# Kernel tuning notes

Hardware: AMD Instinct MI355X
Metric: run time of the kernel (lower is better)

## Reference

```python
import jax, jax.numpy as jnp
import numpy as np


def _conv3x3(x, w, stride=1):
    # x: [N, C_in, H, W], w: [C_out, C_in, 3, 3] (ternary {-1,0,1}), padding=1, no bias
    return jax.lax.conv_general_dilated(
        x, w,
        window_strides=(stride, stride),
        padding=((1, 1), (1, 1)),
        dimension_numbers=("NCHW", "OIHW", "NCHW"),
    )


def _bn(x, gamma, beta, mean, var, eps=1e-5):
    # inference-mode BatchNorm2d over channel dim
    inv = gamma * jax.lax.rsqrt(var + eps)
    return x * inv[None, :, None, None] + (beta - mean * inv)[None, :, None, None]


def setup_inputs() -> dict:
    key = jax.random.key(0)
    ks = jax.random.split(key, 8)
    N, C, H, W = 64, 256, 32, 32
    x = jax.random.normal(ks[0], (N, C, H, W), dtype=jnp.float32)
    # Ternary conv weights in {-1, 0, +1} (scale_and_shift=False => raw ternary values)
    w1 = jax.random.randint(ks[1], (C, C, 3, 3), -1, 2).astype(jnp.float32)
    w2 = jax.random.randint(ks[2], (C, C, 3, 3), -1, 2).astype(jnp.float32)
    # BatchNorm affine params and running stats
    g1 = jax.random.normal(ks[3], (C,), dtype=jnp.float32) * 0.1 + 1.0
    b1 = jax.random.normal(ks[4], (C,), dtype=jnp.float32) * 0.1
    g2 = jax.random.normal(ks[5], (C,), dtype=jnp.float32) * 0.1 + 1.0
    b2 = jax.random.normal(ks[6], (C,), dtype=jnp.float32) * 0.1
    rm1 = jnp.zeros((C,), dtype=jnp.float32)
    rv1 = jnp.ones((C,), dtype=jnp.float32)
    rm2 = jnp.zeros((C,), dtype=jnp.float32)
    rv2 = jnp.ones((C,), dtype=jnp.float32)
    return {"x": x, "w1": w1, "g1": g1, "b1": b1, "rm1": rm1, "rv1": rv1,
            "w2": w2, "g2": g2, "b2": b2, "rm2": rm2, "rv2": rv2}


def reference(x, w1, g1, b1, rm1, rv1, w2, g2, b2, rm2, rv2):
    # BasicBlock forward: stride=1, downsample=None -> identity skip
    h = _conv3x3(x, w1, stride=1)
    h = _bn(h, g1, b1, rm1, rv1)
    h = jax.nn.relu(h)
    h = _conv3x3(h, w2, stride=1)
    h = _bn(h, g2, b2, rm2, rv2)
    return jax.nn.relu(x + h)
```

## Files before the change

### kernel.cpp

```cpp
#include <hip/hip_runtime.h>

typedef unsigned short u16;
typedef unsigned int u32;
typedef __attribute__((ext_vector_type(8))) short bf16x8;
typedef __attribute__((ext_vector_type(4))) float f32x4;

__device__ __forceinline__ u16 f2bf(float f) {
    u32 u = __float_as_uint(f);
    u += 0x7fffu + ((u >> 16) & 1u);
    return (u16)(u >> 16);
}

__device__ __forceinline__ void llds16(void* l, const void* g) {
    __builtin_amdgcn_global_load_lds(
        (const __attribute__((address_space(1))) u32*)g,
        (__attribute__((address_space(3))) u32*)l, 16, 0, 0);
}

__global__ void prep(const float* __restrict__ x, u16* __restrict__ xt,
                     const float* __restrict__ w1, const float* __restrict__ w2,
                     u16* __restrict__ W1t, u16* __restrict__ W2t,
                     const float* __restrict__ g1, const float* __restrict__ b1,
                     const float* __restrict__ rm1, const float* __restrict__ rv1,
                     const float* __restrict__ g2, const float* __restrict__ b2,
                     const float* __restrict__ rm2, const float* __restrict__ rv2,
                     float* __restrict__ sc, u32* __restrict__ zp) {
    int t = threadIdx.x;
    int b = blockIdx.x;
    if (b < 16384) {
        __shared__ float xl[32 * 33];
        int n = b >> 8, rem = b & 255;
        int h = rem >> 3, c0 = (rem & 7) << 5;
        int cl = t >> 5, w = t & 31;
#pragma unroll
        for (int i = 0; i < 4; ++i) {
            int c = c0 + i * 8 + cl;
            xl[(i * 8 + cl) * 33 + w] = x[(n * 256 + c) * 1024 + h * 32 + w];
        }
        __syncthreads();
        int wo = t >> 3, k = t & 7;
        ushort4 o;
        o.x = f2bf(xl[(k * 4 + 0) * 33 + wo]);
        o.y = f2bf(xl[(k * 4 + 1) * 33 + wo]);
        o.z = f2bf(xl[(k * 4 + 2) * 33 + wo]);
        o.w = f2bf(xl[(k * 4 + 3) * 33 + wo]);
        *(ushort4*)&xt[((n * 32 + h) * 32 + wo) * 256 + c0 + k * 4] = o;
    } else {
        int bb = b - 16384;
        int idx = (bb & 255) * 256 + t;
        const float* src = (bb >> 8) ? w2 : w1;
        u16* dst = (bb >> 8) ? W2t : W1t;
        const float* s = src + idx * 9;
        int co = idx >> 8, ci = idx & 255;
#pragma unroll
        for (int p = 0; p < 9; ++p)
            dst[p * 65536 + co * 256 + ci] = f2bf(s[p]);
        if (bb == 0) {
            float s1 = g1[t] * rsqrtf(rv1[t] + 1e-5f);
            sc[t]       = s1;
            sc[256 + t] = b1[t] - rm1[t] * s1;
            float s2 = g2[t] * rsqrtf(rv2[t] + 1e-5f);
            sc[512 + t] = s2;
            sc[768 + t] = b2[t] - rm2[t] * s2;
            zp[t] = 0u;
            zp[t + 256] = 0u;
        }
    }
}

__global__ __launch_bounds__(256, 1) void conv_mfma(
    const u16* __restrict__ Xt,
    const u16* __restrict__ Wt,
    const float* __restrict__ sv,
    const float* __restrict__ tv,
    const float* __restrict__ skip,
    u16* __restrict__ ybf,
    float* __restrict__ yf,
    const u16* __restrict__ zp, int stage)
{
    __shared__ alignas(16) u16 ldsA[2][9 * 4 * 64 * 8];
    __shared__ alignas(16) u16 ldsB[2][40 * 64 * 8];

    int t = threadIdx.x;
    int wv = t >> 6, lane = t & 63;
    int q = lane >> 4, n16 = lane & 15;

    int bid = blockIdx.x;
    int co_t = (bid >> 3) & 3;
    int sp   = ((bid >> 5) << 3) | (bid & 7);
    int h_t  = sp & 1, nb = sp >> 1;
    int co0 = co_t << 6, h0 = h_t << 4;

    const u16* aSrc[9];
#pragma unroll
    for (int i = 0; i < 9; ++i) {
        int g = wv * 9 + i;
        int p = g >> 2, mt = g & 3;
        aSrc[i] = Wt + (p << 16) + ((co0 + (mt << 4) + n16) << 8) + (q << 3);
    }
    const u16* bSrc[10];
#pragma unroll
    for (int j = 0; j < 10; ++j) {
        int g2 = wv * 10 + j;
        int s = g2 * 64 + lane;
        int hi = s / 136, rem = s - hi * 136;
        int wp = rem >> 2, qq = rem & 3;
        int hin = h0 - 1 + hi;
        bool v = (wp >= 1) && (wp <= 32) && (hin >= 0) && (hin < 32);
        bSrc[j] = v ? (Xt + (((nb << 5) + hin) * 32 + (wp - 1)) * 256 + (qq << 3))
                    : (zp + lane * 8);
    }

    f32x4 acc[4][8] = {};

#pragma unroll
    for (int i = 0; i < 9; ++i)
        llds16(&ldsA[0][(wv * 9 + i) << 9], aSrc[i]);
#pragma unroll
    for (int j = 0; j < 10; ++j)
        llds16(&ldsB[0][(wv * 10 + j) << 9], bSrc[j]);

    int c = 0;
    for (int kt = 0; kt < 8; ++kt) {
        if (kt < 7) {
            int kc = (kt + 1) << 5;
#pragma unroll
            for (int i = 0; i < 9; ++i)
                llds16(&ldsA[c ^ 1][(wv * 9 + i) << 9], aSrc[i] + kc);
#pragma unroll
            for (int j = 0; j < 10; ++j)
                llds16(&ldsB[c ^ 1][(wv * 10 + j) << 9], bSrc[j] + kc);
            asm volatile("s_waitcnt vmcnt(19)" ::: "memory");
        } else {
            asm volatile("s_waitcnt vmcnt(0)" ::: "memory");
        }
        __builtin_amdgcn_s_barrier();
        __builtin_amdgcn_sched_barrier(0);

        const u16* pA = ldsA[c];
        const u16* pB = ldsB[c];
        __builtin_amdgcn_s_setprio(1);
#pragma unroll
        for (int kw = 0; kw < 3; ++kw) {
            bf16x8 bFr[6][2];
#pragma unroll
            for (int r = 0; r < 6; ++r)
#pragma unroll
                for (int half = 0; half < 2; ++half) {
                    int hi = (wv << 2) + r;
                    int wp = (half << 4) + n16 + kw;
                    bFr[r][half] = *(const bf16x8*)
                        &pB[(hi * 136 + (wp << 2) + q) << 3];
                }
#pragma unroll
            for (int kh = 0; kh < 3; ++kh) {
                int p = kh * 3 + kw;
                bf16x8 aF[4];
#pragma unroll
                for (int mt = 0; mt < 4; ++mt)
                    aF[mt] = *(const bf16x8*)&pA[((p << 8) + (mt << 6) + lane) << 3];
#pragma unroll
                for (int mt = 0; mt < 4; ++mt)
#pragma unroll
                    for (int nt = 0; nt < 8; ++nt)
                        acc[mt][nt] = __builtin_amdgcn_mfma_f32_16x16x32_bf16(
                            aF[mt], bFr[(nt >> 1) + kh][nt & 1], acc[mt][nt], 0, 0, 0);
            }
        }
        __builtin_amdgcn_s_setprio(0);
        __builtin_amdgcn_sched_barrier(0);
        __builtin_amdgcn_s_barrier();
        c ^= 1;
    }

    if (stage == 1) {
#pragma unroll
        for (int mt = 0; mt < 4; ++mt) {
            int cb = co0 + (mt << 4) + (q << 2);
            f32x4 ss = *(const f32x4*)&sv[cb];
            f32x4 tt = *(const f32x4*)&tv[cb];
#pragma unroll
            for (int nt = 0; nt < 8; ++nt) {
                int h = h0 + (wv << 2) + (nt >> 1), w = ((nt & 1) << 4) + n16;
                ushort4 o;
                o.x = f2bf(fmaxf(acc[mt][nt][0] * ss[0] + tt[0], 0.f));
                o.y = f2bf(fmaxf(acc[mt][nt][1] * ss[1] + tt[1], 0.f));
                o.z = f2bf(fmaxf(acc[mt][nt][2] * ss[2] + tt[2], 0.f));
                o.w = f2bf(fmaxf(acc[mt][nt][3] * ss[3] + tt[3], 0.f));
                *(ushort4*)&ybf[(((nb << 5) + h) * 32 + w) * 256 + cb] = o;
            }
        }
    } else {
#pragma unroll
        for (int mt = 0; mt < 4; ++mt) {
            int cb = co0 + (mt << 4) + (q << 2);
            f32x4 ss = *(const f32x4*)&sv[cb];
            f32x4 tt = *(const f32x4*)&tv[cb];
#pragma unroll
            for (int nt = 0; nt < 8; ++nt) {
                int h = h0 + (wv << 2) + (nt >> 1), w = ((nt & 1) << 4) + n16;
#pragma unroll
                for (int j = 0; j < 4; ++j) {
                    int idx = (((nb << 8) + cb + j) << 10) + (h << 5) + w;
                    yf[idx] = fmaxf(acc[mt][nt][j] * ss[j] + tt[j] + skip[idx], 0.f);
                }
            }
        }
    }
}

extern "C" void kernel_launch(void* const* d_in, const int* in_sizes, int n_in,
                              void* d_out, int out_size, void* d_ws, size_t ws_size,
                              hipStream_t stream) {
    const float* x   = (const float*)d_in[0];
    const float* w1  = (const float*)d_in[1];
    const float* g1  = (const float*)d_in[2];
    const float* b1  = (const float*)d_in[3];
    const float* rm1 = (const float*)d_in[4];
    const float* rv1 = (const float*)d_in[5];
    const float* w2  = (const float*)d_in[6];
    const float* g2  = (const float*)d_in[7];
    const float* b2  = (const float*)d_in[8];
    const float* rm2 = (const float*)d_in[9];
    const float* rv2 = (const float*)d_in[10];

    char* ws = (char*)d_ws;
    u16*  XT  = (u16*)(ws);
    u16*  H1  = (u16*)(ws + 33554432);
    u16*  W1t = (u16*)(ws + 67108864);
    u16*  W2t = (u16*)(ws + 68288512);
    float* sc = (float*)(ws + 69468160);
    u32*  zpg = (u32*)(ws + 69472256);
    if (ws_size < 69474304) return;

    prep<<<16896, 256, 0, stream>>>(x, XT, w1, w2, W1t, W2t,
                                    g1, b1, rm1, rv1, g2, b2, rm2, rv2,
                                    sc, zpg);

    conv_mfma<<<512, 256, 0, stream>>>(XT, W1t, sc, sc + 256, nullptr,
                                       H1, nullptr, (const u16*)zpg, 1);
    conv_mfma<<<512, 256, 0, stream>>>(H1, W2t, sc + 512, sc + 768, x,
                                       nullptr, (float*)d_out, (const u16*)zpg, 2);
}
```

Measured before the change: 306.7 us.

## Double waves per conv block and split global-to-LDS loads by wave role

Each conv block now runs 512 threads (8 waves) in place of 256. Every wave covers 2 output rows instead of 4, which halves the accumulator array and the B-fragment registers per wave. The global-to-LDS copies are split by role: waves 0-3 load the input tile (10 loads each) and waves 4-7 load the weight tile (9 loads each), with the vmcnt waits adjusted to match. The aim is more waves to hide latency and fewer registers per wave. The cost is more barrier participants, and the A fragments are now loaded from LDS twice as often relative to the MFMA work.

```diff
diff --git a/kernel.cpp b/kernel.cpp
--- a/kernel.cpp
+++ b/kernel.cpp
@@ -68,7 +68,7 @@
     }
 }
 
-__global__ __launch_bounds__(256, 1) void conv_mfma(
+__global__ __launch_bounds__(512, 1) void conv_mfma(
     const u16* __restrict__ Xt,
     const u16* __restrict__ Wt,
     const float* __restrict__ sv,
@@ -91,46 +91,53 @@
     int h_t  = sp & 1, nb = sp >> 1;
     int co0 = co_t << 6, h0 = h_t << 4;
 
-    const u16* aSrc[9];
-#pragma unroll
-    for (int i = 0; i < 9; ++i) {
-        int g = wv * 9 + i;
-        int p = g >> 2, mt = g & 3;
-        aSrc[i] = Wt + (p << 16) + ((co0 + (mt << 4) + n16) << 8) + (q << 3);
-    }
-    const u16* bSrc[10];
-#pragma unroll
-    for (int j = 0; j < 10; ++j) {
-        int g2 = wv * 10 + j;
-        int s = g2 * 64 + lane;
-        int hi = s / 136, rem = s - hi * 136;
-        int wp = rem >> 2, qq = rem & 3;
-        int hin = h0 - 1 + hi;
-        bool v = (wp >= 1) && (wp <= 32) && (hin >= 0) && (hin < 32);
-        bSrc[j] = v ? (Xt + (((nb << 5) + hin) * 32 + (wp - 1)) * 256 + (qq << 3))
-                    : (zp + lane * 8);
-    }
-
-    f32x4 acc[4][8] = {};
-
-#pragma unroll
-    for (int i = 0; i < 9; ++i)
-        llds16(&ldsA[0][(wv * 9 + i) << 9], aSrc[i]);
-#pragma unroll
-    for (int j = 0; j < 10; ++j)
-        llds16(&ldsB[0][(wv * 10 + j) << 9], bSrc[j]);
+    const u16* src[10];
+    u32 dstOff[10];
+    bool isB = (wv < 4);
+    int nld = isB ? 10 : 9;
+    if (isB) {
+#pragma unroll
+        for (int j = 0; j < 10; ++j) {
+            int g2 = wv * 10 + j;
+            int s = g2 * 64 + lane;
+            int hi = s / 136, rem = s - hi * 136;
+            int wp = rem >> 2, qq = rem & 3;
+            int hin = h0 - 1 + hi;
+            bool v = (wp >= 1) && (wp <= 32) && (hin >= 0) && (hin < 32);
+            src[j] = v ? (Xt + (((nb << 5) + hin) * 32 + (wp - 1)) * 256 + (qq << 3))
+                       : (zp + lane * 8);
+            dstOff[j] = (u32)g2 << 9;
+        }
+    } else {
+#pragma unroll
+        for (int i = 0; i < 9; ++i) {
+            int g = (wv - 4) * 9 + i;
+            int p = g >> 2, mt = g & 3;
+            src[i] = Wt + (p << 16) + ((co0 + (mt << 4) + n16) << 8) + (q << 3);
+            dstOff[i] = (u32)g << 9;
+        }
+        src[9] = zp; dstOff[9] = 0;
+    }
+
+    f32x4 acc[4][4] = {};
+
+    {
+        u16* dst = isB ? ldsB[0] : ldsA[0];
+#pragma unroll
+        for (int j = 0; j < 10; ++j)
+            if (j < nld) llds16(&dst[dstOff[j]], src[j]);
+    }
 
     int c = 0;
     for (int kt = 0; kt < 8; ++kt) {
         if (kt < 7) {
             int kc = (kt + 1) << 5;
-#pragma unroll
-            for (int i = 0; i < 9; ++i)
-                llds16(&ldsA[c ^ 1][(wv * 9 + i) << 9], aSrc[i] + kc);
+            u16* dst = isB ? ldsB[c ^ 1] : ldsA[c ^ 1];
 #pragma unroll
             for (int j = 0; j < 10; ++j)
-                llds16(&ldsB[c ^ 1][(wv * 10 + j) << 9], bSrc[j] + kc);
-            asm volatile("s_waitcnt vmcnt(19)" ::: "memory");
+                if (j < nld) llds16(&dst[dstOff[j]], src[j] + kc);
+            if (isB) asm volatile("s_waitcnt vmcnt(10)" ::: "memory");
+            else     asm volatile("s_waitcnt vmcnt(9)"  ::: "memory");
         } else {
             asm volatile("s_waitcnt vmcnt(0)" ::: "memory");
         }
@@ -142,12 +149,12 @@
         __builtin_amdgcn_s_setprio(1);
 #pragma unroll
         for (int kw = 0; kw < 3; ++kw) {
-            bf16x8 bFr[6][2];
-#pragma unroll
-            for (int r = 0; r < 6; ++r)
+            bf16x8 bFr[4][2];
+#pragma unroll
+            for (int r = 0; r < 4; ++r)
 #pragma unroll
                 for (int half = 0; half < 2; ++half) {
-                    int hi = (wv << 2) + r;
+                    int hi = (wv << 1) + r;
                     int wp = (half << 4) + n16 + kw;
                     bFr[r][half] = *(const bf16x8*)
                         &pB[(hi * 136 + (wp << 2) + q) << 3];
@@ -162,7 +169,7 @@
 #pragma unroll
                 for (int mt = 0; mt < 4; ++mt)
 #pragma unroll
-                    for (int nt = 0; nt < 8; ++nt)
+                    for (int nt = 0; nt < 4; ++nt)
                         acc[mt][nt] = __builtin_amdgcn_mfma_f32_16x16x32_bf16(
                             aF[mt], bFr[(nt >> 1) + kh][nt & 1], acc[mt][nt], 0, 0, 0);
             }
@@ -180,8 +187,8 @@
             f32x4 ss = *(const f32x4*)&sv[cb];
             f32x4 tt = *(const f32x4*)&tv[cb];
 #pragma unroll
-            for (int nt = 0; nt < 8; ++nt) {
-                int h = h0 + (wv << 2) + (nt >> 1), w = ((nt & 1) << 4) + n16;
+            for (int nt = 0; nt < 4; ++nt) {
+                int h = h0 + (wv << 1) + (nt >> 1), w = ((nt & 1) << 4) + n16;
                 ushort4 o;
                 o.x = f2bf(fmaxf(acc[mt][nt][0] * ss[0] + tt[0], 0.f));
                 o.y = f2bf(fmaxf(acc[mt][nt][1] * ss[1] + tt[1], 0.f));
@@ -197,8 +204,8 @@
             f32x4 ss = *(const f32x4*)&sv[cb];
             f32x4 tt = *(const f32x4*)&tv[cb];
 #pragma unroll
-            for (int nt = 0; nt < 8; ++nt) {
-                int h = h0 + (wv << 2) + (nt >> 1), w = ((nt & 1) << 4) + n16;
+            for (int nt = 0; nt < 4; ++nt) {
+                int h = h0 + (wv << 1) + (nt >> 1), w = ((nt & 1) << 4) + n16;
 #pragma unroll
                 for (int j = 0; j < 4; ++j) {
                     int idx = (((nb << 8) + cb + j) << 10) + (h << 5) + w;
@@ -237,8 +244,8 @@
                                     g1, b1, rm1, rv1, g2, b2, rm2, rv2,
                                     sc, zpg);
 
-    conv_mfma<<<512, 256, 0, stream>>>(XT, W1t, sc, sc + 256, nullptr,
+    conv_mfma<<<512, 512, 0, stream>>>(XT, W1t, sc, sc + 256, nullptr,
                                        H1, nullptr, (const u16*)zpg, 1);
-    conv_mfma<<<512, 256, 0, stream>>>(H1, W2t, sc + 512, sc + 768, x,
+    conv_mfma<<<512, 512, 0, stream>>>(H1, W2t, sc + 512, sc + 768, x,
                                        nullptr, (float*)d_out, (const u16*)zpg, 2);
 }
```

New measurement: 272.6 us. 11.1% less time.

## Use full-height 512-thread tiles with wave-specialized A/B loaders

Applied to the files above, without the earlier changes.

Each block now computes all 32 output rows of one image for 64 output channels with 8 waves, which halves the grid and cuts redundant halo loads of the input tile. Waves 0-3 load weights (double-buffered) and waves 4-7 load the activation tile. The activation tile is single-buffered: the kw=2 fragments are prefetched into registers so the next chunk can be loaded mid-iteration. The risks are weaker load/compute overlap from the vmcnt(0) wait at the top of each iteration, and register pressure. Launch bounds of (512,2) may cap VGPRs low enough to spill the 128-float accumulator.

```diff
diff --git a/kernel.cpp b/kernel.cpp
--- a/kernel.cpp
+++ b/kernel.cpp
@@ -68,7 +68,7 @@
     }
 }
 
-__global__ __launch_bounds__(256, 1) void conv_mfma(
+__global__ __launch_bounds__(512, 2) void conv_mfma(
     const u16* __restrict__ Xt,
     const u16* __restrict__ Wt,
     const float* __restrict__ sv,
@@ -79,7 +79,7 @@
     const u16* __restrict__ zp, int stage)
 {
     __shared__ alignas(16) u16 ldsA[2][9 * 4 * 64 * 8];
-    __shared__ alignas(16) u16 ldsB[2][40 * 64 * 8];
+    __shared__ alignas(16) u16 ldsB[73 * 512];
 
     int t = threadIdx.x;
     int wv = t >> 6, lane = t & 63;
@@ -87,78 +87,79 @@
 
     int bid = blockIdx.x;
     int co_t = (bid >> 3) & 3;
-    int sp   = ((bid >> 5) << 3) | (bid & 7);
-    int h_t  = sp & 1, nb = sp >> 1;
-    int co0 = co_t << 6, h0 = h_t << 4;
-
-    const u16* aSrc[9];
-#pragma unroll
-    for (int i = 0; i < 9; ++i) {
-        int g = wv * 9 + i;
-        int p = g >> 2, mt = g & 3;
-        aSrc[i] = Wt + (p << 16) + ((co0 + (mt << 4) + n16) << 8) + (q << 3);
-    }
-    const u16* bSrc[10];
-#pragma unroll
-    for (int j = 0; j < 10; ++j) {
-        int g2 = wv * 10 + j;
-        int s = g2 * 64 + lane;
-        int hi = s / 136, rem = s - hi * 136;
-        int wp = rem >> 2, qq = rem & 3;
-        int hin = h0 - 1 + hi;
-        bool v = (wp >= 1) && (wp <= 32) && (hin >= 0) && (hin < 32);
-        bSrc[j] = v ? (Xt + (((nb << 5) + hin) * 32 + (wp - 1)) * 256 + (qq << 3))
-                    : (zp + lane * 8);
+    int n = (bid & 7) | ((bid >> 5) << 3);
+    int co0 = co_t << 6;
+
+    bool isA = (wv < 4);
+    u32 srcOff[19];
+    if (isA) {
+#pragma unroll
+        for (int i = 0; i < 9; ++i) {
+            int g = wv * 9 + i;
+            int p = g >> 2, mt = g & 3;
+            srcOff[i] = (u32)((p << 16) + ((co0 + (mt << 4) + n16) << 8) + (q << 3));
+        }
+    } else {
+        u32 zpOff = (u32)((const u16*)zp - Xt);
+#pragma unroll
+        for (int j = 0; j < 19; ++j) {
+            int g2 = (wv - 4) + 4 * j;
+            int s = g2 * 64 + lane;
+            int hi = s / 136, rem = s - hi * 136;
+            int wp = rem >> 2, qq = rem & 3;
+            int h = hi - 1, w = wp - 1;
+            bool v = (s < 4624) && (h >= 0) && (h < 32) && (w >= 0) && (w < 32);
+            srcOff[j] = v ? (u32)(((n * 32 + h) * 32 + w) * 256 + (qq << 3))
+                          : (zpOff + lane * 8);
+        }
     }
 
     f32x4 acc[4][8] = {};
 
-#pragma unroll
-    for (int i = 0; i < 9; ++i)
-        llds16(&ldsA[0][(wv * 9 + i) << 9], aSrc[i]);
-#pragma unroll
-    for (int j = 0; j < 10; ++j)
-        llds16(&ldsB[0][(wv * 10 + j) << 9], bSrc[j]);
+    if (isA) {
+#pragma unroll
+        for (int i = 0; i < 9; ++i)
+            llds16((char*)&ldsA[0][0] + (((u32)(wv * 9 + i)) << 10), Xt ? (Wt + srcOff[i]) : 0);
+    } else {
+#pragma unroll
+        for (int j = 0; j < 18; ++j)
+            llds16((char*)ldsB + (((u32)((wv - 4) + 4 * j)) << 10), Xt + srcOff[j]);
+        if (wv == 4)
+            llds16((char*)ldsB + (72u << 10), Xt + srcOff[18]);
+    }
 
     int c = 0;
     for (int kt = 0; kt < 8; ++kt) {
-        if (kt < 7) {
-            int kc = (kt + 1) << 5;
+        asm volatile("s_waitcnt vmcnt(0)" ::: "memory");
+        __builtin_amdgcn_s_barrier();
+
+        const u16* pA = ldsA[c];
+        int kc1 = (kt + 1) << 5;
+        if (kt < 7 && isA) {
 #pragma unroll
             for (int i = 0; i < 9; ++i)
-                llds16(&ldsA[c ^ 1][(wv * 9 + i) << 9], aSrc[i] + kc);
-#pragma unroll
-            for (int j = 0; j < 10; ++j)
-                llds16(&ldsB[c ^ 1][(wv * 10 + j) << 9], bSrc[j] + kc);
-            asm volatile("s_waitcnt vmcnt(19)" ::: "memory");
-        } else {
-            asm volatile("s_waitcnt vmcnt(0)" ::: "memory");
-        }
-        __builtin_amdgcn_s_barrier();
+                llds16((char*)&ldsA[c ^ 1][0] + (((u32)(wv * 9 + i)) << 10),
+                       Wt + srcOff[i] + kc1);
+        }
         __builtin_amdgcn_sched_barrier(0);
 
-        const u16* pA = ldsA[c];
-        const u16* pB = ldsB[c];
-        __builtin_amdgcn_s_setprio(1);
-#pragma unroll
-        for (int kw = 0; kw < 3; ++kw) {
+#pragma unroll
+        for (int kw = 0; kw < 2; ++kw) {
             bf16x8 bFr[6][2];
 #pragma unroll
-            for (int r = 0; r < 6; ++r)
-#pragma unroll
-                for (int half = 0; half < 2; ++half) {
-                    int hi = (wv << 2) + r;
-                    int wp = (half << 4) + n16 + kw;
-                    bFr[r][half] = *(const bf16x8*)
-                        &pB[(hi * 136 + (wp << 2) + q) << 3];
-                }
+            for (int rr = 0; rr < 6; ++rr)
+#pragma unroll
+                for (int half = 0; half < 2; ++half)
+                    bFr[rr][half] = *(const bf16x8*)
+                        &ldsB[(((wv * 4 + rr) * 34 + (half * 16 + n16 + kw)) * 4 + q) * 8];
+            __builtin_amdgcn_s_setprio(1);
 #pragma unroll
             for (int kh = 0; kh < 3; ++kh) {
                 int p = kh * 3 + kw;
                 bf16x8 aF[4];
 #pragma unroll
                 for (int mt = 0; mt < 4; ++mt)
-                    aF[mt] = *(const bf16x8*)&pA[((p << 8) + (mt << 6) + lane) << 3];
+                    aF[mt] = *(const bf16x8*)&pA[((p * 4 + mt) * 64 + lane) * 8];
 #pragma unroll
                 for (int mt = 0; mt < 4; ++mt)
 #pragma unroll
@@ -166,10 +167,46 @@
                         acc[mt][nt] = __builtin_amdgcn_mfma_f32_16x16x32_bf16(
                             aF[mt], bFr[(nt >> 1) + kh][nt & 1], acc[mt][nt], 0, 0, 0);
             }
-        }
-        __builtin_amdgcn_s_setprio(0);
+            __builtin_amdgcn_s_setprio(0);
+        }
+
+        bf16x8 bF2[6][2];
+#pragma unroll
+        for (int rr = 0; rr < 6; ++rr)
+#pragma unroll
+            for (int half = 0; half < 2; ++half)
+                bF2[rr][half] = *(const bf16x8*)
+                    &ldsB[(((wv * 4 + rr) * 34 + (half * 16 + n16 + 2)) * 4 + q) * 8];
+        asm volatile("s_waitcnt lgkmcnt(0)" ::: "memory");
         __builtin_amdgcn_sched_barrier(0);
         __builtin_amdgcn_s_barrier();
+
+        if (kt < 7 && !isA) {
+#pragma unroll
+            for (int j = 0; j < 18; ++j)
+                llds16((char*)ldsB + (((u32)((wv - 4) + 4 * j)) << 10),
+                       Xt + srcOff[j] + kc1);
+            if (wv == 4)
+                llds16((char*)ldsB + (72u << 10), Xt + srcOff[18] + kc1);
+        }
+        __builtin_amdgcn_sched_barrier(0);
+
+        __builtin_amdgcn_s_setprio(1);
+#pragma unroll
+        for (int kh = 0; kh < 3; ++kh) {
+            int p = kh * 3 + 2;
+            bf16x8 aF[4];
+#pragma unroll
+            for (int mt = 0; mt < 4; ++mt)
+                aF[mt] = *(const bf16x8*)&pA[((p * 4 + mt) * 64 + lane) * 8];
+#pragma unroll
+            for (int mt = 0; mt < 4; ++mt)
+#pragma unroll
+                for (int nt = 0; nt < 8; ++nt)
+                    acc[mt][nt] = __builtin_amdgcn_mfma_f32_16x16x32_bf16(
+                        aF[mt], bF2[(nt >> 1) + kh][nt & 1], acc[mt][nt], 0, 0, 0);
+        }
+        __builtin_amdgcn_s_setprio(0);
         c ^= 1;
     }
 
@@ -181,13 +218,13 @@
             f32x4 tt = *(const f32x4*)&tv[cb];
 #pragma unroll
             for (int nt = 0; nt < 8; ++nt) {
-                int h = h0 + (wv << 2) + (nt >> 1), w = ((nt & 1) << 4) + n16;
+                int h = (wv << 2) + (nt >> 1), w = ((nt & 1) << 4) + n16;
                 ushort4 o;
                 o.x = f2bf(fmaxf(acc[mt][nt][0] * ss[0] + tt[0], 0.f));
                 o.y = f2bf(fmaxf(acc[mt][nt][1] * ss[1] + tt[1], 0.f));
                 o.z = f2bf(fmaxf(acc[mt][nt][2] * ss[2] + tt[2], 0.f));
                 o.w = f2bf(fmaxf(acc[mt][nt][3] * ss[3] + tt[3], 0.f));
-                *(ushort4*)&ybf[(((nb << 5) + h) * 32 + w) * 256 + cb] = o;
+                *(ushort4*)&ybf[((n * 32 + h) * 32 + w) * 256 + cb] = o;
             }
         }
     } else {
@@ -198,10 +235,10 @@
             f32x4 tt = *(const f32x4*)&tv[cb];
 #pragma unroll
             for (int nt = 0; nt < 8; ++nt) {
-                int h = h0 + (wv << 2) + (nt >> 1), w = ((nt & 1) << 4) + n16;
+                int h = (wv << 2) + (nt >> 1), w = ((nt & 1) << 4) + n16;
 #pragma unroll
                 for (int j = 0; j < 4; ++j) {
-                    int idx = (((nb << 8) + cb + j) << 10) + (h << 5) + w;
+                    int idx = (((n << 8) + cb + j) << 10) + (h << 5) + w;
                     yf[idx] = fmaxf(acc[mt][nt][j] * ss[j] + tt[j] + skip[idx], 0.f);
                 }
             }
@@ -237,8 +274,8 @@
                                     g1, b1, rm1, rv1, g2, b2, rm2, rv2,
                                     sc, zpg);
 
-    conv_mfma<<<512, 256, 0, stream>>>(XT, W1t, sc, sc + 256, nullptr,
+    conv_mfma<<<256, 512, 0, stream>>>(XT, W1t, sc, sc + 256, nullptr,
                                        H1, nullptr, (const u16*)zpg, 1);
-    conv_mfma<<<512, 256, 0, stream>>>(H1, W2t, sc + 512, sc + 768, x,
+    conv_mfma<<<256, 512, 0, stream>>>(H1, W2t, sc + 512, sc + 768, x,
                                        nullptr, (float*)d_out, (const u16*)zpg, 2);
 }
```

After: 322.3 us. 1.05x slower.
